# Performance work log

Measured on AMD Instinct MI355X. Metric: run time of the kernel, lower is better.

The kernel has to match this reference:

```python
import jax, jax.numpy as jnp
import numpy as np

ALPHA = 0.5
DECAY = 0.5
THR = 0.5

B, T, N_IN, N_HID = 64, 256, 128, 2048


def setup_inputs() -> dict:
    key = jax.random.key(0)
    k1, k2, k3, k4, k5 = jax.random.split(key, 5)
    x = jax.random.normal(k1, (B, T, N_IN), dtype=jnp.float32)
    W_in = jax.random.uniform(k2, (N_IN, N_HID), minval=-0.1, maxval=0.1, dtype=jnp.float32)
    A = jax.random.uniform(k3, (N_HID, N_HID), minval=-0.1, maxval=0.1, dtype=jnp.float32)
    bias = jax.random.uniform(k4, (N_HID,), minval=-1.0, maxval=1.0, dtype=jnp.float32)
    mem0 = jax.random.uniform(k5, (B, N_HID), minval=0.0, maxval=0.2, dtype=jnp.float32)
    return {"x": x, "W_in": W_in, "A": A, "bias": bias, "mem0": mem0}


def reference(x, W_in, A, bias, mem0):
    # x: [B, T, N_in] -> outputs mems, spikes: [1, B, T, N_hid]
    spike0 = jnp.zeros_like(mem0)

    def step(carry, x_t):
        mem, spike = carry
        U = x_t @ W_in                      # [B, N_hid]
        r = spike @ A                       # [B, N_hid]
        y = jnp.tanh(ALPHA * r + (1.0 - ALPHA) * (U + bias))
        mem = mem * DECAY - THR * (1.0 - spike) + y
        spike = (mem > THR).astype(jnp.float32)
        return (mem, spike), (mem, spike)

    xs = jnp.swapaxes(x, 0, 1)              # [T, B, N_in]
    _, (mems_t, spikes_t) = jax.lax.scan(step, (mem0, spike0), xs)
    mems = jnp.swapaxes(mems_t, 0, 1)[None]     # [1, B, T, N_hid]
    spikes = jnp.swapaxes(spikes_t, 0, 1)[None]  # [1, B, T, N_hid]
    return mems, spikes
```

## Files before the change

### kernel.cpp

```cpp
#include <hip/hip_runtime.h>
#include <math.h>

#define B_   64
#define T_   256
#define NIN  128
#define NH   2048
#define NTHR 512

typedef unsigned int  u32;
typedef unsigned short u16;
typedef unsigned long long u64;
typedef __attribute__((ext_vector_type(8))) short bf16x8;
typedef __attribute__((ext_vector_type(4))) float f32x4;
typedef __attribute__((ext_vector_type(4))) u32   u32x4;

#define OFF_AHI  0
#define OFF_ALO  65792
#define OFF_CRED 131584
#define SMEM_BYTES 148992


__device__ __forceinline__ u16 f2bf(float f) {
    u32 u = __float_as_uint(f);
    return (u16)((u + 0x7FFFu + ((u >> 16) & 1u)) >> 16);
}
__device__ __forceinline__ float bf2f(u16 h) { return __uint_as_float(((u32)h) << 16); }

__device__ __forceinline__ float zthrf_of(float c) {
    if (c >= 1.f)  return  __builtin_inff();
    if (c <= -1.f) return -__builtin_inff();
    return 0.5f * logf((1.f + c) / (1.f - c));
}

__global__ __launch_bounds__(256, 2) void u_init(
    const float* __restrict__ x, const float* __restrict__ W_in,
    const float* __restrict__ bias, float* __restrict__ u_out)
{
    __shared__ float xS[32 * 132];
    const int tid = threadIdx.x, bid = blockIdx.x;
    const int row0 = bid * 32;
    for (int idx = tid; idx < 32 * NIN; idx += 256) {
        int r = idx >> 7, k = idx & 127;
        xS[r * 132 + k] = x[(size_t)(row0 + r) * NIN + k];
    }
    __syncthreads();

    float bc[4][2];
#pragma unroll
    for (int cg = 0; cg < 2; ++cg)
#pragma unroll
        for (int q = 0; q < 4; ++q)
            bc[q][cg] = bias[cg * 1024 + q * 256 + tid];

    for (int cg = 0; cg < 2; ++cg) {
        for (int rg = 0; rg < 2; ++rg) {
            float acc[4][16];
#pragma unroll
            for (int q = 0; q < 4; ++q)
#pragma unroll
                for (int r = 0; r < 16; ++r) acc[q][r] = 0.f;
            for (int kc = 0; kc < 8; ++kc) {
                float w[4][16];
#pragma unroll
                for (int q = 0; q < 4; ++q)
#pragma unroll
                    for (int kk = 0; kk < 16; ++kk)
                        w[q][kk] = W_in[(size_t)(kc * 16 + kk) * NH + cg * 1024 + q * 256 + tid];
#pragma unroll
                for (int r = 0; r < 16; ++r) {
                    const f32x4* xv = (const f32x4*)(xS + (rg * 16 + r) * 132 + kc * 16);
#pragma unroll
                    for (int v = 0; v < 4; ++v) {
                        f32x4 xx = xv[v];
#pragma unroll
                        for (int q = 0; q < 4; ++q) {
                            acc[q][r] = fmaf(xx.x, w[q][v * 4 + 0], acc[q][r]);
                            acc[q][r] = fmaf(xx.y, w[q][v * 4 + 1], acc[q][r]);
                            acc[q][r] = fmaf(xx.z, w[q][v * 4 + 2], acc[q][r]);
                            acc[q][r] = fmaf(xx.w, w[q][v * 4 + 3], acc[q][r]);
                        }
                    }
                }
            }
#pragma unroll
            for (int r = 0; r < 16; ++r)
#pragma unroll
                for (int q = 0; q < 4; ++q)
                    u_out[(size_t)(row0 + rg * 16 + r) * NH + cg * 1024 + q * 256 + tid]
                        = 0.5f * (acc[q][r] + bc[q][cg]);
        }
    }
}

__global__ __launch_bounds__(NTHR, 2) void persist(
    const float* __restrict__ A,
    const float* __restrict__ mem0,
    float* __restrict__ out_mem,
    float* out_spk,
    u32* __restrict__ spkbuf)
{
    extern __shared__ char smem[];
    u16*   AhiS = (u16*)(smem + OFF_AHI);
    u16*   AloS = (u16*)(smem + OFF_ALO);
    float* cred = (float*)(smem + OFF_CRED);

    const int tid = threadIdx.x;
    const int bid = blockIdx.x;
    const int cb  = bid & 127;
    const int bg  = bid >> 7;
    const int c0  = cb * 16;

    for (int idx = tid; idx < NH * 16; idx += NTHR) {
        int i = idx >> 4, c = idx & 15;
        float a = A[(size_t)i * NH + c0 + c];
        u16 hi = f2bf(a);
        AhiS[c * 2056 + i] = hi;
        AloS[c * 2056 + i] = f2bf(a - bf2f(hi));
    }

    const int n   = tid & 15;
    const int bl  = tid >> 4;
    const int b   = bg * 32 + bl;
    const int col = c0 + n;
    double m = (double)mem0[(size_t)b * NH + col];
    double sprev = 0.0;
    float zthrf = zthrf_of((float)(1.0 - 0.5 * m));

    const int lane = tid & 63, wave = tid >> 6;
    const int qn = lane & 15, quad = lane >> 4;
    const int mt = wave & 1;
    const int kp = wave >> 1;
    const u32 sh = ((u32)(quad & 1) * 8) + ((u32)(quad >> 1) * 16);

    float up = out_spk[(size_t)b * T_ * NH + col];

    u32* stgW = (u32*)smem + wave * 320;

    const u32* pollbase = spkbuf
        + (size_t)(bg * 32 + mt * 16 + (lane >> 2)) * 128 + kp * 32 + (lane & 3) * 8;

    __syncthreads();

    bf16x8 Ah[16], Al[16];
#pragma unroll
    for (int ktl = 0; ktl < 16; ++ktl) {
        int kt = kp * 16 + ktl;
        Ah[ktl] = *(const bf16x8*)(AhiS + qn * 2056 + quad * 8 + kt * 32);
        Al[ktl] = *(const bf16x8*)(AloS + qn * 2056 + quad * 8 + kt * 32);
    }
#pragma unroll
    for (int i = 0; i < 16; ++i)
        asm volatile("" : "+v"(Ah[i]), "+v"(Al[i]));

    __syncthreads();

    for (int t = 0; t < T_; ++t) {
        float upn = 0.f;
        if (t + 1 < T_) upn = out_spk[((size_t)b * T_ + t + 1) * NH + col];

        const u32* src = pollbase + ((t & 1) ? 8192 : 0);
        const u32 te = (u32)t << 16;
        u32x4 da, db;
        int guard = 0;
        while (true) {
            asm volatile(
                "global_load_dwordx4 %0, %2, off sc1\n\t"
                "global_load_dwordx4 %1, %2, off offset:16 sc1\n\t"
                "s_waitcnt vmcnt(0)"
                : "=&v"(da), "=&v"(db)
                : "v"(src)
                : "memory");
            u32 bad = (da.x ^ te) | (da.y ^ te) | (da.z ^ te) | (da.w ^ te)
                    | (db.x ^ te) | (db.y ^ te) | (db.z ^ te) | (db.w ^ te);
            if (!(bad >> 16)) break;
            if (++guard > 30000) break;
            if (guard > 1) __builtin_amdgcn_s_sleep(1);
        }
        u32x4 pk;
        pk.x = (da.x & 0xFFFFu) | (da.y << 16);
        pk.y = (da.z & 0xFFFFu) | (da.w << 16);
        pk.z = (db.x & 0xFFFFu) | (db.y << 16);
        pk.w = (db.z & 0xFFFFu) | (db.w << 16);
        *(u32x4*)(stgW + (lane >> 2) * 20 + (lane & 3) * 4) = pk;
        asm volatile("s_waitcnt lgkmcnt(0)" ::: "memory");

        u32 sw[16];
        {
            const u32x4* rp = (const u32x4*)(stgW + qn * 20);
            u32x4 s0 = rp[0], s1 = rp[1], s2 = rp[2], s3 = rp[3];
            sw[0] = s0.x; sw[1] = s0.y; sw[2]  = s0.z; sw[3]  = s0.w;
            sw[4] = s1.x; sw[5] = s1.y; sw[6]  = s1.z; sw[7]  = s1.w;
            sw[8] = s2.x; sw[9] = s2.y; sw[10] = s2.z; sw[11] = s2.w;
            sw[12] = s3.x; sw[13] = s3.y; sw[14] = s3.z; sw[15] = s3.w;
        }

        f32x4 acc = {0.f, 0.f, 0.f, 0.f};
#pragma unroll
        for (int ktl = 0; ktl < 16; ++ktl) {
            u32 byte = (sw[ktl] >> sh) & 255u;
            u32x4 aw;
            aw.x = ((byte & 1u)   ? 0x3F80u : 0u) | ((byte & 2u)   ? 0x3F800000u : 0u);
            aw.y = ((byte & 4u)   ? 0x3F80u : 0u) | ((byte & 8u)   ? 0x3F800000u : 0u);
            aw.z = ((byte & 16u)  ? 0x3F80u : 0u) | ((byte & 32u)  ? 0x3F800000u : 0u);
            aw.w = ((byte & 64u)  ? 0x3F80u : 0u) | ((byte & 128u) ? 0x3F800000u : 0u);
            bf16x8 af = __builtin_bit_cast(bf16x8, aw);
            acc = __builtin_amdgcn_mfma_f32_16x16x32_bf16(af, Ah[ktl], acc, 0, 0, 0);
            acc = __builtin_amdgcn_mfma_f32_16x16x32_bf16(af, Al[ktl], acc, 0, 0, 0);
        }
        float* cw = cred + (t & 1) * 2176;
#pragma unroll
        for (int reg = 0; reg < 4; ++reg)
            cw[((kp * 2 + mt) * 16 + quad * 4 + reg) * 17 + qn] = acc[reg];
        __syncthreads();

        float r = 0.f;
#pragma unroll
        for (int p = 0; p < 4; ++p)
            r += cw[((p * 2 + (bl >> 4)) * 16 + (bl & 15)) * 17 + n];

        float zf = 0.5f * r + up;
        int sp = zf > zthrf;

        u64 bal = __ballot(sp);
        if (n == 0) {
            u32 bits = (u32)((bal >> ((bl & 3) * 16)) & 0xFFFFull);
            u32 val = ((u32)(t + 1) << 16) | bits;
            u32* dst = spkbuf + ((t & 1) ? 0 : 8192) + b * 128 + cb;
            __hip_atomic_store(dst, val, __ATOMIC_RELAXED, __HIP_MEMORY_SCOPE_AGENT);
        }

        float y = tanhf(zf);
        m = m * 0.5 - 0.5 * (1.0 - sprev) + (double)y;
        size_t o = ((size_t)b * T_ + t) * NH + col;
        out_mem[o] = (float)m;
        out_spk[o] = sp ? 1.f : 0.f;
        sprev = sp ? 1.0 : 0.0;
        zthrf = zthrf_of((float)(1.0 - 0.5 * m - 0.5 * sprev));
        up = upn;
    }
}

extern "C" void kernel_launch(void* const* d_in, const int* in_sizes, int n_in,
                              void* d_out, int out_size, void* d_ws, size_t ws_size,
                              hipStream_t stream) {
    const float* x    = (const float*)d_in[0];
    const float* W_in = (const float*)d_in[1];
    const float* A    = (const float*)d_in[2];
    const float* bias = (const float*)d_in[3];
    const float* mem0 = (const float*)d_in[4];

    float* out_mem = (float*)d_out;
    float* out_spk = out_mem + (size_t)B_ * T_ * NH;
    u32*   spkbuf  = (u32*)d_ws;

    (void)hipFuncSetAttribute((const void*)persist,
                              hipFuncAttributeMaxDynamicSharedMemorySize, SMEM_BYTES);

    hipMemsetAsync(spkbuf, 0, 2 * 64 * 128 * sizeof(u32), stream);
    hipLaunchKernelGGL(u_init, dim3(512), dim3(256), 0, stream, x, W_in, bias, out_spk);
    hipLaunchKernelGGL(persist, dim3(256), dim3(NTHR), SMEM_BYTES, stream,
                       A, mem0, out_mem, out_spk, spkbuf);
}
```

Measured before the change: 1.310 ms.

## Prefetch next-step spike poll early and split MFMA accumulation chains

The persistent recurrent kernel now issues the global poll load for the next timestep's spike buffer right after publishing its own spikes, so that load overlaps with the tanh/membrane update and output stores. The wait and check happen at the top of the next iteration, with retries only if the data is stale. The MFMA chain is split into four independent accumulators to break the serial dependency, and the u_init precompute is restructured with fewer registers and higher occupancy. An early poll that returns stale data can add an extra round trip, and the extra accumulators use more registers.

```diff
diff --git a/kernel.cpp b/kernel.cpp
--- a/kernel.cpp
+++ b/kernel.cpp
@@ -32,7 +32,14 @@
     return 0.5f * logf((1.f + c) / (1.f - c));
 }
 
-__global__ __launch_bounds__(256, 2) void u_init(
+#define ISSUE_POLL(s, A_, B_)                                         \
+    asm volatile("global_load_dwordx4 %0, %2, off sc1\n\t"            \
+                 "global_load_dwordx4 %1, %2, off offset:16 sc1"      \
+                 : "=&v"(A_), "=&v"(B_) : "v"(s) : "memory")
+#define WAIT_POLL(A_, B_)                                             \
+    asm volatile("s_waitcnt vmcnt(0)" : "+v"(A_), "+v"(B_) :: "memory")
+
+__global__ __launch_bounds__(256, 4) void u_init(
     const float* __restrict__ x, const float* __restrict__ W_in,
     const float* __restrict__ bias, float* __restrict__ u_out)
 {
@@ -45,49 +52,40 @@
     }
     __syncthreads();
 
-    float bc[4][2];
-#pragma unroll
-    for (int cg = 0; cg < 2; ++cg)
-#pragma unroll
-        for (int q = 0; q < 4; ++q)
-            bc[q][cg] = bias[cg * 1024 + q * 256 + tid];
-
-    for (int cg = 0; cg < 2; ++cg) {
+    for (int cg = 0; cg < 4; ++cg) {
+        const int c0 = cg * 512 + tid;
+        const float b0 = bias[c0], b1 = bias[c0 + 256];
         for (int rg = 0; rg < 2; ++rg) {
-            float acc[4][16];
-#pragma unroll
-            for (int q = 0; q < 4; ++q)
-#pragma unroll
-                for (int r = 0; r < 16; ++r) acc[q][r] = 0.f;
+            float acc0[16], acc1[16];
+#pragma unroll
+            for (int r = 0; r < 16; ++r) { acc0[r] = 0.f; acc1[r] = 0.f; }
             for (int kc = 0; kc < 8; ++kc) {
-                float w[4][16];
-#pragma unroll
-                for (int q = 0; q < 4; ++q)
-#pragma unroll
-                    for (int kk = 0; kk < 16; ++kk)
-                        w[q][kk] = W_in[(size_t)(kc * 16 + kk) * NH + cg * 1024 + q * 256 + tid];
+                float w0[16], w1[16];
+#pragma unroll
+                for (int kk = 0; kk < 16; ++kk) {
+                    w0[kk] = W_in[(size_t)(kc * 16 + kk) * NH + c0];
+                    w1[kk] = W_in[(size_t)(kc * 16 + kk) * NH + c0 + 256];
+                }
 #pragma unroll
                 for (int r = 0; r < 16; ++r) {
                     const f32x4* xv = (const f32x4*)(xS + (rg * 16 + r) * 132 + kc * 16);
+                    float a0 = acc0[r], a1 = acc1[r];
 #pragma unroll
                     for (int v = 0; v < 4; ++v) {
                         f32x4 xx = xv[v];
-#pragma unroll
-                        for (int q = 0; q < 4; ++q) {
-                            acc[q][r] = fmaf(xx.x, w[q][v * 4 + 0], acc[q][r]);
-                            acc[q][r] = fmaf(xx.y, w[q][v * 4 + 1], acc[q][r]);
-                            acc[q][r] = fmaf(xx.z, w[q][v * 4 + 2], acc[q][r]);
-                            acc[q][r] = fmaf(xx.w, w[q][v * 4 + 3], acc[q][r]);
-                        }
+                        a0 = fmaf(xx.x, w0[v * 4 + 0], a0); a1 = fmaf(xx.x, w1[v * 4 + 0], a1);
+                        a0 = fmaf(xx.y, w0[v * 4 + 1], a0); a1 = fmaf(xx.y, w1[v * 4 + 1], a1);
+                        a0 = fmaf(xx.z, w0[v * 4 + 2], a0); a1 = fmaf(xx.z, w1[v * 4 + 2], a1);
+                        a0 = fmaf(xx.w, w0[v * 4 + 3], a0); a1 = fmaf(xx.w, w1[v * 4 + 3], a1);
                     }
+                    acc0[r] = a0; acc1[r] = a1;
                 }
             }
 #pragma unroll
-            for (int r = 0; r < 16; ++r)
-#pragma unroll
-                for (int q = 0; q < 4; ++q)
-                    u_out[(size_t)(row0 + rg * 16 + r) * NH + cg * 1024 + q * 256 + tid]
-                        = 0.5f * (acc[q][r] + bc[q][cg]);
+            for (int r = 0; r < 16; ++r) {
+                u_out[(size_t)(row0 + rg * 16 + r) * NH + c0]       = 0.5f * (acc0[r] + b0);
+                u_out[(size_t)(row0 + rg * 16 + r) * NH + c0 + 256] = 0.5f * (acc1[r] + b1);
+            }
         }
     }
 }
@@ -154,28 +152,29 @@
 
     __syncthreads();
 
+    const u32* src = pollbase;
+    u32x4 da, db;
+    ISSUE_POLL(src, da, db);
+
     for (int t = 0; t < T_; ++t) {
+        const u32 te = (u32)t << 16;
+
+        WAIT_POLL(da, db);
+        u32 bad = (da.x ^ te) | (da.y ^ te) | (da.z ^ te) | (da.w ^ te)
+                | (db.x ^ te) | (db.y ^ te) | (db.z ^ te) | (db.w ^ te);
+        int guard = 0;
+        while (bad >> 16) {
+            if (++guard > 30000) break;
+            if (guard > 2) __builtin_amdgcn_s_sleep(1);
+            ISSUE_POLL(src, da, db);
+            WAIT_POLL(da, db);
+            bad = (da.x ^ te) | (da.y ^ te) | (da.z ^ te) | (da.w ^ te)
+                | (db.x ^ te) | (db.y ^ te) | (db.z ^ te) | (db.w ^ te);
+        }
+
         float upn = 0.f;
         if (t + 1 < T_) upn = out_spk[((size_t)b * T_ + t + 1) * NH + col];
 
-        const u32* src = pollbase + ((t & 1) ? 8192 : 0);
-        const u32 te = (u32)t << 16;
-        u32x4 da, db;
-        int guard = 0;
-        while (true) {
-            asm volatile(
-                "global_load_dwordx4 %0, %2, off sc1\n\t"
-                "global_load_dwordx4 %1, %2, off offset:16 sc1\n\t"
-                "s_waitcnt vmcnt(0)"
-                : "=&v"(da), "=&v"(db)
-                : "v"(src)
-                : "memory");
-            u32 bad = (da.x ^ te) | (da.y ^ te) | (da.z ^ te) | (da.w ^ te)
-                    | (db.x ^ te) | (db.y ^ te) | (db.z ^ te) | (db.w ^ te);
-            if (!(bad >> 16)) break;
-            if (++guard > 30000) break;
-            if (guard > 1) __builtin_amdgcn_s_sleep(1);
-        }
         u32x4 pk;
         pk.x = (da.x & 0xFFFFu) | (da.y << 16);
         pk.y = (da.z & 0xFFFFu) | (da.w << 16);
@@ -194,19 +193,26 @@
             sw[12] = s3.x; sw[13] = s3.y; sw[14] = s3.z; sw[15] = s3.w;
         }
 
-        f32x4 acc = {0.f, 0.f, 0.f, 0.f};
-#pragma unroll
-        for (int ktl = 0; ktl < 16; ++ktl) {
-            u32 byte = (sw[ktl] >> sh) & 255u;
-            u32x4 aw;
-            aw.x = ((byte & 1u)   ? 0x3F80u : 0u) | ((byte & 2u)   ? 0x3F800000u : 0u);
-            aw.y = ((byte & 4u)   ? 0x3F80u : 0u) | ((byte & 8u)   ? 0x3F800000u : 0u);
-            aw.z = ((byte & 16u)  ? 0x3F80u : 0u) | ((byte & 32u)  ? 0x3F800000u : 0u);
-            aw.w = ((byte & 64u)  ? 0x3F80u : 0u) | ((byte & 128u) ? 0x3F800000u : 0u);
-            bf16x8 af = __builtin_bit_cast(bf16x8, aw);
-            acc = __builtin_amdgcn_mfma_f32_16x16x32_bf16(af, Ah[ktl], acc, 0, 0, 0);
-            acc = __builtin_amdgcn_mfma_f32_16x16x32_bf16(af, Al[ktl], acc, 0, 0, 0);
-        }
+        f32x4 ac0 = {0.f,0.f,0.f,0.f}, ac1 = {0.f,0.f,0.f,0.f};
+        f32x4 ac2 = {0.f,0.f,0.f,0.f}, ac3 = {0.f,0.f,0.f,0.f};
+#pragma unroll
+        for (int ktl = 0; ktl < 4; ++ktl) {
+#pragma unroll
+            for (int c = 0; c < 4; ++c) {
+                int k = c * 4 + ktl;
+                u32 byte = (sw[k] >> sh) & 255u;
+                u32x4 aw;
+                aw.x = ((byte & 1u)   ? 0x3F80u : 0u) | ((byte & 2u)   ? 0x3F800000u : 0u);
+                aw.y = ((byte & 4u)   ? 0x3F80u : 0u) | ((byte & 8u)   ? 0x3F800000u : 0u);
+                aw.z = ((byte & 16u)  ? 0x3F80u : 0u) | ((byte & 32u)  ? 0x3F800000u : 0u);
+                aw.w = ((byte & 64u)  ? 0x3F80u : 0u) | ((byte & 128u) ? 0x3F800000u : 0u);
+                bf16x8 af = __builtin_bit_cast(bf16x8, aw);
+                f32x4* ac = (c == 0) ? &ac0 : (c == 1) ? &ac1 : (c == 2) ? &ac2 : &ac3;
+                *ac = __builtin_amdgcn_mfma_f32_16x16x32_bf16(af, Ah[k], *ac, 0, 0, 0);
+                *ac = __builtin_amdgcn_mfma_f32_16x16x32_bf16(af, Al[k], *ac, 0, 0, 0);
+            }
+        }
+        f32x4 acc = (ac0 + ac1) + (ac2 + ac3);
         float* cw = cred + (t & 1) * 2176;
 #pragma unroll
         for (int reg = 0; reg < 4; ++reg)
@@ -228,6 +234,9 @@
             u32* dst = spkbuf + ((t & 1) ? 0 : 8192) + b * 128 + cb;
             __hip_atomic_store(dst, val, __ATOMIC_RELAXED, __HIP_MEMORY_SCOPE_AGENT);
         }
+
+        src = pollbase + (((t + 1) & 1) ? 8192 : 0);
+        if (t + 1 < T_) ISSUE_POLL(src, da, db);
 
         float y = tanhf(zf);
         m = m * 0.5 - 0.5 * (1.0 - sprev) + (double)y;
```

Result: slower. 3.441 ms (+162.7%).
